# Kernel tuning notes

Measured on AMD Instinct MI355X. Metric: run time of the kernel, lower is better.

## Reference

```python
import jax, jax.numpy as jnp
import numpy as np
import math

B, T, C, H = 2, 2048, 1024, 16

def setup_inputs() -> dict:
    key = jax.random.key(0)
    ks = jax.random.split(key, 5)
    s = 0.02
    return {
        "x": jax.random.normal(ks[0], (B, T, C), dtype=jnp.float32),
        "W_attn": jax.random.normal(ks[1], (C, 3 * C), dtype=jnp.float32) * s,
        "b_attn": jnp.zeros((3 * C,), dtype=jnp.float32),
        "W_proj": jax.random.normal(ks[2], (C, C), dtype=jnp.float32) * s,
        "b_proj": jnp.zeros((C,), dtype=jnp.float32),
    }

def reference(x, W_attn, b_attn, W_proj, b_proj):
    Bx, Tx, Cx = x.shape
    hd = Cx // H  # head dim = 64
    qkv = x @ W_attn + b_attn                      # [B,T,3C]
    q, k, v = jnp.split(qkv, 3, axis=-1)
    # [B,H,T,hd]
    q = q.reshape(Bx, Tx, H, hd).transpose(0, 2, 1, 3)
    k = k.reshape(Bx, Tx, H, hd).transpose(0, 2, 1, 3)
    v = v.reshape(Bx, Tx, H, hd).transpose(0, 2, 1, 3)
    scale = 1.0 / math.sqrt(hd)
    att = jnp.einsum('bhqd,bhkd->bhqk', q, k) * scale   # [B,H,T,T]
    causal = jnp.tril(jnp.ones((Tx, Tx), dtype=bool))
    att = jnp.where(causal[None, None, :, :], att, -jnp.inf)
    att = jax.nn.softmax(att, axis=-1)
    y = jnp.einsum('bhqk,bhkd->bhqd', att, v)           # [B,H,T,hd]
    y = y.transpose(0, 2, 1, 3).reshape(Bx, Tx, Cx)
    return y @ W_proj + b_proj
```

## Files before the change

### kernel.cpp

```cpp
#include <hip/hip_runtime.h>

typedef __attribute__((ext_vector_type(8))) __bf16 bf16x8;
typedef __attribute__((ext_vector_type(4))) float f32x4;

#define T_SEQ 2048
#define NH 16
#define HD 64
#define CDIM 1024
#define NQK 2048
#define NQKV 3072
#define MTOT 4096

#define SWZ(r, c) ((((r) * 8) + ((c) ^ ((r) & 7))) * 8)

__device__ __forceinline__ void async_load16(const void* g, void* l) {
    __builtin_amdgcn_global_load_lds(
        (const __attribute__((address_space(1))) void*)g,
        (__attribute__((address_space(3))) void*)l, 16, 0, 0);
}

__device__ __forceinline__ unsigned cvtpk_bf16(float lo, float hi) {
    unsigned r;
    asm("v_cvt_pk_bf16_f32 %0, %1, %2" : "=v"(r) : "v"(lo), "v"(hi));
    return r;
}
__device__ __forceinline__ void swap32(unsigned& a, unsigned& b) {
    asm("v_permlane32_swap_b32 %0, %1" : "+v"(a), "+v"(b));
}
__device__ __forceinline__ void swap16(unsigned& a, unsigned& b) {
    asm("v_permlane16_swap_b32 %0, %1" : "+v"(a), "+v"(b));
}

__global__ __launch_bounds__(256) void cvt_bf16_kernel(const float* __restrict__ in,
                                                       __bf16* __restrict__ out, int n) {
    int i = (blockIdx.x * 256 + threadIdx.x) * 8;
    if (i + 8 <= n) {
        float4 f0 = *(const float4*)(in + i);
        float4 f1 = *(const float4*)(in + i + 4);
        bf16x8 o;
        o[0] = (__bf16)f0.x; o[1] = (__bf16)f0.y; o[2] = (__bf16)f0.z; o[3] = (__bf16)f0.w;
        o[4] = (__bf16)f1.x; o[5] = (__bf16)f1.y; o[6] = (__bf16)f1.z; o[7] = (__bf16)f1.w;
        *(bf16x8*)(out + i) = o;
    }
}

__global__ __launch_bounds__(256) void transpose2_kernel(
    const float* __restrict__ Wa, const float* __restrict__ Wp,
    __bf16* __restrict__ WaT, __bf16* __restrict__ WpT) {
    __shared__ float tile[32][33];
    const float* in; __bf16* out; int C, bx = blockIdx.x;
    if (bx < 96) { in = Wa; out = WaT; C = 3072; }
    else         { in = Wp; out = WpT; C = 1024; bx -= 96; }
    int c0 = bx * 32, r0 = blockIdx.y * 32;
    int tx = threadIdx.x, ty = threadIdx.y;
#pragma unroll
    for (int i = 0; i < 4; i++)
        tile[ty + i * 8][tx] = in[(size_t)(r0 + ty + i * 8) * C + c0 + tx];
    __syncthreads();
#pragma unroll
    for (int i = 0; i < 4; i++)
        out[(size_t)(c0 + ty + i * 8) * 1024 + r0 + tx] = (__bf16)tile[tx][ty + i * 8];
}

template <int WNW>
__global__ __launch_bounds__(256) void gemm_bt_kernel(
    const __bf16* __restrict__ A, const __bf16* __restrict__ Bt,
    const float* __restrict__ bias, int M, int N, int K, int mode,
    __bf16* __restrict__ qkb, __bf16* __restrict__ vtb, float* __restrict__ outf)
{
    constexpr int MI = (WNW == 2) ? 4 : 2;
    constexpr int BROWS = WNW * 64;
    __shared__ __bf16 As[128 * 64];
    __shared__ __bf16 Bs[BROWS * 64];

    int tid = threadIdx.x;
    int lane = tid & 63, wid = tid >> 6;
    int quad = lane >> 4, r16 = lane & 15;
    int wm = (WNW == 2) ? (wid >> 1) * 64 : wid * 32;
    int wn = (WNW == 2) ? (wid & 1) * 64 : 0;
    int bm = blockIdx.y * 128, bn = blockIdx.x * (WNW * 64);

    f32x4 acc[MI][4] = {};

    int lrow = lane >> 3;
    int lcolsw = (((lane & 7) ^ (lrow & 7)) * 8);
    const __bf16* Ag = A + (size_t)(bm + wid * 32 + lrow) * K + lcolsw;
    const __bf16* Bg = Bt + (size_t)(bn + wid * (BROWS / 4) + lrow) * K + lcolsw;
    char* lA = (char*)As + wid * 4096;
    char* lB = (char*)Bs + wid * (BROWS / 4) * 128;

    for (int kt = 0; kt < K; kt += 64) {
        __syncthreads();
#pragma unroll
        for (int i = 0; i < 4; i++)
            async_load16(Ag + kt + (size_t)i * 8 * K, lA + i * 1024);
#pragma unroll
        for (int i = 0; i < BROWS / 32; i++)
            async_load16(Bg + kt + (size_t)i * 8 * K, lB + i * 1024);
        __syncthreads();
#pragma unroll
        for (int ks = 0; ks < 2; ks++) {
            bf16x8 af[MI], bfr[4];
#pragma unroll
            for (int i = 0; i < MI; i++)
                af[i] = *(const bf16x8*)&As[SWZ(wm + i * 16 + r16, ks * 4 + quad)];
#pragma unroll
            for (int i = 0; i < 4; i++)
                bfr[i] = *(const bf16x8*)&Bs[SWZ(wn + i * 16 + r16, ks * 4 + quad)];
#pragma unroll
            for (int mi = 0; mi < MI; mi++)
#pragma unroll
                for (int ni = 0; ni < 4; ni++)
                    acc[mi][ni] = __builtin_amdgcn_mfma_f32_16x16x32_bf16(
                        af[mi], bfr[ni], acc[mi][ni], 0, 0, 0);
        }
    }

    const float SC2 = 0.125f * 1.44269504088896f;
#pragma unroll
    for (int mi = 0; mi < MI; mi++) {
#pragma unroll
        for (int ni = 0; ni < 4; ni++) {
            int col = bn + wn + ni * 16 + r16;
            float bv = bias[col];
            int row0 = bm + wm + mi * 16 + quad * 4;
            if (mode == 1) {
#pragma unroll
                for (int rg = 0; rg < 4; rg++)
                    outf[(size_t)(row0 + rg) * N + col] = acc[mi][ni][rg] + bv;
            } else if (col < 1024) {
#pragma unroll
                for (int rg = 0; rg < 4; rg++)
                    qkb[(size_t)(row0 + rg) * NQK + col] = (__bf16)((acc[mi][ni][rg] + bv) * SC2);
            } else if (col < 2048) {
#pragma unroll
                for (int rg = 0; rg < 4; rg++)
                    qkb[(size_t)(row0 + rg) * NQK + col] = (__bf16)(acc[mi][ni][rg] + bv);
            } else {
                int dcol = col - 2048;
                int b = row0 >> 11, t0 = row0 & 2047;
                union { __bf16 h[4]; uint2 u; } pk;
#pragma unroll
                for (int rg = 0; rg < 4; rg++) pk.h[rg] = (__bf16)(acc[mi][ni][rg] + bv);
                *(uint2*)&vtb[((size_t)b * 1024 + dcol) * T_SEQ + t0] = pk.u;
            }
        }
    }
}

__global__ __launch_bounds__(256) void attn_kernel(
    const __bf16* __restrict__ qkb, const __bf16* __restrict__ vtb,
    __bf16* __restrict__ y1)
{
    __shared__ __bf16 Ks[2][64 * 64];
    __shared__ __bf16 Vs[2][64 * 64];

    int tid = threadIdx.x;
    int lane = tid & 63, w = tid >> 6;
    int quad = lane >> 4, r16 = lane & 15;
    int bh = blockIdx.y;
    int b = bh >> 4, h = bh & 15;
    int qtA = blockIdx.x, qtB = 31 - blockIdx.x;
    int qbA = qtA * 64, qbB = qtB * 64;

    const __bf16* Qh = qkb + (size_t)b * T_SEQ * NQK + h * HD;
    const __bf16* Kh = Qh + CDIM;
    const __bf16* Vh = vtb + ((size_t)b * 1024 + h * HD) * T_SEQ;

    const float NEG_INF = -__builtin_inff();
    int lrow = lane >> 3;
    int lcolsw = (((lane & 7) ^ (lrow & 7)) * 8);

    bf16x8 qfA[2], qfB[2];
#pragma unroll
    for (int ks = 0; ks < 2; ks++) {
        qfA[ks] = *(const bf16x8*)(Qh + (size_t)(qbA + w * 16 + r16) * NQK + ks * 32 + quad * 8);
        qfB[ks] = *(const bf16x8*)(Qh + (size_t)(qbB + w * 16 + r16) * NQK + ks * 32 + quad * 8);
    }

    bf16x8 onesv;
#pragma unroll
    for (int i = 0; i < 8; i++) onesv[i] = (__bf16)1.0f;

    f32x4 oA[4] = {}, oB[4] = {};
    f32x4 lA4 = {}, lB4 = {};
    int g0A = qbA + w * 16, g0B = qbB + w * 16;
    int qrowA = g0A + r16, qrowB = g0B + r16;

    auto stage = [&](int kt, int buf) {
        int kb = kt * 64;
        char* lK = (char*)Ks[buf] + w * 2048;
        char* lV = (char*)Vs[buf] + w * 2048;
        const __bf16* kg = Kh + (size_t)(kb + w * 16 + lrow) * NQK + lcolsw;
        const __bf16* vg = Vh + (size_t)(w * 16 + lrow) * T_SEQ + kb + lcolsw;
        async_load16(kg, lK);
        async_load16(kg + (size_t)8 * NQK, lK + 1024);
        async_load16(vg, lV);
        async_load16(vg + (size_t)8 * T_SEQ, lV + 1024);
    };

    auto softmax_xchg = [&](f32x4 (&s)[4], int qrow, int kb, bool diag,
                            bf16x8 (&pb)[2]) {
        if (diag) {
#pragma unroll
            for (int ni = 0; ni < 4; ni++)
#pragma unroll
                for (int rg = 0; rg < 4; rg++)
                    if (kb + ni * 16 + quad * 4 + rg > qrow) s[ni][rg] = NEG_INF;
        }
#pragma unroll
        for (int ni = 0; ni < 4; ni++)
#pragma unroll
            for (int rg = 0; rg < 4; rg++)
                s[ni][rg] = __builtin_amdgcn_exp2f(s[ni][rg]);
#pragma unroll
        for (int ks = 0; ks < 2; ks++) {
            unsigned X0 = cvtpk_bf16(s[2 * ks][0], s[2 * ks][1]);
            unsigned X1 = cvtpk_bf16(s[2 * ks][2], s[2 * ks][3]);
            unsigned Y0 = cvtpk_bf16(s[2 * ks + 1][0], s[2 * ks + 1][1]);
            unsigned Y1 = cvtpk_bf16(s[2 * ks + 1][2], s[2 * ks + 1][3]);
            swap32(X0, Y0); swap16(X0, Y0);
            swap32(X1, Y1); swap16(X1, Y1);
            union { unsigned u[4]; bf16x8 v; } pk;
            pk.u[0] = X0; pk.u[1] = X1; pk.u[2] = Y0; pk.u[3] = Y1;
            pb[ks] = pk.v;
        }
    };

    int nktA = qtA + 1, nktB = qtB + 1;
    stage(0, 0);
    int cur = 0;
    for (int kt = 0; kt < nktB; kt++) {
        __syncthreads();
        if (kt + 1 < nktB) stage(kt + 1, cur ^ 1);
        const bool doA = (kt < nktA);
        const int kb = kt * 64;

        f32x4 sB[4] = {}, sA[4] = {};
#pragma unroll
        for (int ks = 0; ks < 2; ks++) {
            bf16x8 kf[4];
#pragma unroll
            for (int ni = 0; ni < 4; ni++)
                kf[ni] = *(const bf16x8*)&Ks[cur][SWZ(ni * 16 + r16, ks * 4 + quad)];
            __builtin_amdgcn_s_setprio(1);
#pragma unroll
            for (int ni = 0; ni < 4; ni++)
                sB[ni] = __builtin_amdgcn_mfma_f32_16x16x32_bf16(kf[ni], qfB[ks], sB[ni], 0, 0, 0);
            if (doA) {
#pragma unroll
                for (int ni = 0; ni < 4; ni++)
                    sA[ni] = __builtin_amdgcn_mfma_f32_16x16x32_bf16(kf[ni], qfA[ks], sA[ni], 0, 0, 0);
            }
            __builtin_amdgcn_s_setprio(0);
        }

        bf16x8 pbB[2], pbA[2];
        softmax_xchg(sB, qrowB, kb, kb + 63 > g0B, pbB);
        if (doA) softmax_xchg(sA, qrowA, kb, kb + 63 > g0A, pbA);

#pragma unroll
        for (int ks = 0; ks < 2; ks++) {
            bf16x8 vf[4];
#pragma unroll
            for (int nd = 0; nd < 4; nd++)
                vf[nd] = *(const bf16x8*)&Vs[cur][SWZ(nd * 16 + r16, ks * 4 + quad)];
            __builtin_amdgcn_s_setprio(1);
#pragma unroll
            for (int nd = 0; nd < 4; nd++)
                oB[nd] = __builtin_amdgcn_mfma_f32_16x16x32_bf16(vf[nd], pbB[ks], oB[nd], 0, 0, 0);
            lB4 = __builtin_amdgcn_mfma_f32_16x16x32_bf16(onesv, pbB[ks], lB4, 0, 0, 0);
            __builtin_amdgcn_s_setprio(0);
            if (doA) {
                __builtin_amdgcn_s_setprio(1);
#pragma unroll
                for (int nd = 0; nd < 4; nd++)
                    oA[nd] = __builtin_amdgcn_mfma_f32_16x16x32_bf16(vf[nd], pbA[ks], oA[nd], 0, 0, 0);
                lA4 = __builtin_amdgcn_mfma_f32_16x16x32_bf16(onesv, pbA[ks], lA4, 0, 0, 0);
                __builtin_amdgcn_s_setprio(0);
            }
        }
        cur ^= 1;
    }

#pragma unroll
    for (int which = 0; which < 2; which++) {
        f32x4* o = which ? oB : oA;
        float inv = 1.f / (which ? lB4[0] : lA4[0]);
        int t = (which ? qbB : qbA) + w * 16 + r16;
#pragma unroll
        for (int nd = 0; nd < 4; nd++) {
            union { __bf16 h4[4]; uint2 u; } pk;
#pragma unroll
            for (int rg = 0; rg < 4; rg++) pk.h4[rg] = (__bf16)(o[nd][rg] * inv);
            *(uint2*)&y1[(size_t)(b * T_SEQ + t) * CDIM + h * HD + nd * 16 + quad * 4] = pk.u;
        }
    }
}

extern "C" void kernel_launch(void* const* d_in, const int* in_sizes, int n_in,
                              void* d_out, int out_size, void* d_ws, size_t ws_size,
                              hipStream_t stream) {
    const float* x = (const float*)d_in[0];
    const float* W_attn = (const float*)d_in[1];
    const float* b_attn = (const float*)d_in[2];
    const float* W_proj = (const float*)d_in[3];
    const float* b_proj = (const float*)d_in[4];
    float* out = (float*)d_out;

    char* p = (char*)d_ws;
    __bf16* xb = (__bf16*)p;   p += (size_t)MTOT * CDIM * 2;
    __bf16* WaT = (__bf16*)p;  p += (size_t)3 * CDIM * CDIM * 2;
    __bf16* WpT = (__bf16*)p;  p += (size_t)CDIM * CDIM * 2;
    __bf16* qkb = (__bf16*)p;  p += (size_t)MTOT * NQK * 2;
    __bf16* vtb = (__bf16*)p;  p += (size_t)2 * 1024 * T_SEQ * 2;
    __bf16* y1 = xb;

    cvt_bf16_kernel<<<2048, 256, 0, stream>>>(x, xb, MTOT * CDIM);
    transpose2_kernel<<<dim3(128, 32), dim3(32, 8), 0, stream>>>(W_attn, W_proj, WaT, WpT);
    gemm_bt_kernel<2><<<dim3(24, 32), 256, 0, stream>>>(xb, WaT, b_attn, MTOT, NQKV, CDIM, 0,
                                                        qkb, vtb, nullptr);
    attn_kernel<<<dim3(16, 32), 256, 0, stream>>>(qkb, vtb, y1);
    gemm_bt_kernel<1><<<dim3(16, 32), 256, 0, stream>>>(y1, WpT, b_proj, MTOT, CDIM, CDIM, 1,
                                                        nullptr, nullptr, out);
}
```

Before: 182.0 us.

## Software-pipeline attention: overlap previous tile's PV MFMAs with current softmax

Restructures the attention loop so the P·V MFMAs for tile kt-1 run after the QK^T MFMAs of tile kt and before its softmax. The goal is to hide the exp/convert/lane-exchange latency of softmax behind matrix work. K/V shared memory grows from double to triple buffering so the previous V tile stays resident while the next one is prefetched. An epilogue drains the last tile. In exchange, register pressure rises (P fragments are carried across iterations) and LDS use rises to 48KB, which could lower occupancy.

```diff
diff --git a/kernel.cpp b/kernel.cpp
--- a/kernel.cpp
+++ b/kernel.cpp
@@ -152,8 +152,8 @@
     const __bf16* __restrict__ qkb, const __bf16* __restrict__ vtb,
     __bf16* __restrict__ y1)
 {
-    __shared__ __bf16 Ks[2][64 * 64];
-    __shared__ __bf16 Vs[2][64 * 64];
+    __shared__ __bf16 Ks[3][64 * 64];
+    __shared__ __bf16 Vs[3][64 * 64];
 
     int tid = threadIdx.x;
     int lane = tid & 63, w = tid >> 6;
@@ -189,8 +189,8 @@
 
     auto stage = [&](int kt, int buf) {
         int kb = kt * 64;
-        char* lK = (char*)Ks[buf] + w * 2048;
-        char* lV = (char*)Vs[buf] + w * 2048;
+        char* lK = (char*)&Ks[buf][0] + w * 2048;
+        char* lV = (char*)&Vs[buf][0] + w * 2048;
         const __bf16* kg = Kh + (size_t)(kb + w * 16 + lrow) * NQK + lcolsw;
         const __bf16* vg = Vh + (size_t)(w * 16 + lrow) * T_SEQ + kb + lcolsw;
         async_load16(kg, lK);
@@ -229,11 +229,15 @@
 
     int nktA = qtA + 1, nktB = qtB + 1;
     stage(0, 0);
+    bf16x8 pbA_p[2] = {}, pbB_p[2] = {};
     int cur = 0;
     for (int kt = 0; kt < nktB; kt++) {
         __syncthreads();
-        if (kt + 1 < nktB) stage(kt + 1, cur ^ 1);
+        int nxt = cur + 1; if (nxt == 3) nxt = 0;
+        int prv = cur - 1; if (prv < 0) prv = 2;
+        if (kt + 1 < nktB) stage(kt + 1, nxt);
         const bool doA = (kt < nktA);
+        const bool doAp = (kt > 0) & (kt - 1 < nktA);
         const int kb = kt * 64;
 
         f32x4 sB[4] = {}, sA[4] = {};
@@ -255,32 +259,46 @@
             __builtin_amdgcn_s_setprio(0);
         }
 
-        bf16x8 pbB[2], pbA[2];
-        softmax_xchg(sB, qrowB, kb, kb + 63 > g0B, pbB);
-        if (doA) softmax_xchg(sA, qrowA, kb, kb + 63 > g0A, pbA);
-
+        if (kt > 0) {
+#pragma unroll
+            for (int ks = 0; ks < 2; ks++) {
+                bf16x8 vf[4];
+#pragma unroll
+                for (int nd = 0; nd < 4; nd++)
+                    vf[nd] = *(const bf16x8*)&Vs[prv][SWZ(nd * 16 + r16, ks * 4 + quad)];
+                __builtin_amdgcn_s_setprio(1);
+#pragma unroll
+                for (int nd = 0; nd < 4; nd++)
+                    oB[nd] = __builtin_amdgcn_mfma_f32_16x16x32_bf16(vf[nd], pbB_p[ks], oB[nd], 0, 0, 0);
+                lB4 = __builtin_amdgcn_mfma_f32_16x16x32_bf16(onesv, pbB_p[ks], lB4, 0, 0, 0);
+                if (doAp) {
+#pragma unroll
+                    for (int nd = 0; nd < 4; nd++)
+                        oA[nd] = __builtin_amdgcn_mfma_f32_16x16x32_bf16(vf[nd], pbA_p[ks], oA[nd], 0, 0, 0);
+                    lA4 = __builtin_amdgcn_mfma_f32_16x16x32_bf16(onesv, pbA_p[ks], lA4, 0, 0, 0);
+                }
+                __builtin_amdgcn_s_setprio(0);
+            }
+        }
+
+        softmax_xchg(sB, qrowB, kb, kb + 63 > g0B, pbB_p);
+        if (doA) softmax_xchg(sA, qrowA, kb, kb + 63 > g0A, pbA_p);
+        cur = nxt;
+    }
+
+    {
+        int prv = cur - 1; if (prv < 0) prv = 2;
 #pragma unroll
         for (int ks = 0; ks < 2; ks++) {
             bf16x8 vf[4];
 #pragma unroll
             for (int nd = 0; nd < 4; nd++)
-                vf[nd] = *(const bf16x8*)&Vs[cur][SWZ(nd * 16 + r16, ks * 4 + quad)];
-            __builtin_amdgcn_s_setprio(1);
+                vf[nd] = *(const bf16x8*)&Vs[prv][SWZ(nd * 16 + r16, ks * 4 + quad)];
 #pragma unroll
             for (int nd = 0; nd < 4; nd++)
-                oB[nd] = __builtin_amdgcn_mfma_f32_16x16x32_bf16(vf[nd], pbB[ks], oB[nd], 0, 0, 0);
-            lB4 = __builtin_amdgcn_mfma_f32_16x16x32_bf16(onesv, pbB[ks], lB4, 0, 0, 0);
-            __builtin_amdgcn_s_setprio(0);
-            if (doA) {
-                __builtin_amdgcn_s_setprio(1);
-#pragma unroll
-                for (int nd = 0; nd < 4; nd++)
-                    oA[nd] = __builtin_amdgcn_mfma_f32_16x16x32_bf16(vf[nd], pbA[ks], oA[nd], 0, 0, 0);
-                lA4 = __builtin_amdgcn_mfma_f32_16x16x32_bf16(onesv, pbA[ks], lA4, 0, 0, 0);
-                __builtin_amdgcn_s_setprio(0);
-            }
-        }
-        cur ^= 1;
+                oB[nd] = __builtin_amdgcn_mfma_f32_16x16x32_bf16(vf[nd], pbB_p[ks], oB[nd], 0, 0, 0);
+            lB4 = __builtin_amdgcn_mfma_f32_16x16x32_bf16(onesv, pbB_p[ks], lB4, 0, 0, 0);
+        }
     }
 
 #pragma unroll
```

Result: slower. 185.6 us (+2.0%).
